# Kernel tuning notes

Hardware: AMD Instinct MI355X
Metric: run time of the kernel (lower is better)

## Reference

```python
import jax, jax.numpy as jnp
import numpy as np

N, E, D, K = 50000, 800000, 128, 128


def _graph_conv(x, src, dst, w, W_rel, b_rel, W_root, n_nodes):
    # PyG GraphConv (aggr='add'): out = lin_rel(sum_j w_ij * x_j) + lin_root(x)
    msg = w[:, None] * x[src]                              # [E, D]
    agg = jax.ops.segment_sum(msg, dst, num_segments=n_nodes)  # [N, D]
    return agg @ W_rel + b_rel + x @ W_root


def setup_inputs() -> dict:
    key = jax.random.key(0)
    ks = jax.random.split(key, 16)
    sc = 1.0 / np.sqrt(D).astype(np.float32)
    inp = {
        "x": jax.random.normal(ks[0], (N, D), dtype=jnp.float32),
        "edge_index": jax.random.randint(ks[1], (2, E), 0, N, dtype=jnp.int64 if jax.config.jax_enable_x64 else jnp.int32),
        "edge_weight": jax.random.uniform(ks[2], (E,), dtype=jnp.float32),
        # GraphConv layer 1
        "W_rel1": jax.random.normal(ks[3], (D, D), dtype=jnp.float32) * sc,
        "b_rel1": jnp.zeros((D,), dtype=jnp.float32),
        "W_root1": jax.random.normal(ks[4], (D, D), dtype=jnp.float32) * sc,
        # GraphConv layer 2
        "W_rel2": jax.random.normal(ks[5], (D, D), dtype=jnp.float32) * sc,
        "b_rel2": jnp.zeros((D,), dtype=jnp.float32),
        "W_root2": jax.random.normal(ks[6], (D, D), dtype=jnp.float32) * sc,
        # MLP: Linear(D,128) + Identity, then final Linear(128,K)
        "W_m1": jax.random.normal(ks[7], (D, 128), dtype=jnp.float32) * sc,
        "b_m1": jnp.zeros((128,), dtype=jnp.float32),
        "W_out": jax.random.normal(ks[8], (128, K), dtype=jnp.float32) * (1.0 / np.sqrt(128).astype(np.float32)),
        "b_out": jnp.zeros((K,), dtype=jnp.float32),
    }
    return inp


def reference(x, edge_index, edge_weight, W_rel1, b_rel1, W_root1,
              W_rel2, b_rel2, W_root2, W_m1, b_m1, W_out, b_out):
    n_nodes = x.shape[0]
    src, dst = edge_index[0], edge_index[1]

    # Message passing stack with ReLU
    h = jax.nn.relu(_graph_conv(x, src, dst, edge_weight, W_rel1, b_rel1, W_root1, n_nodes))
    h = jax.nn.relu(_graph_conv(h, src, dst, edge_weight, W_rel2, b_rel2, W_root2, n_nodes))

    # MLP -> cluster logits (mlp_act = Identity)
    s = (h @ W_m1 + b_m1) @ W_out + b_out                  # [N, K]
    probs = jax.nn.softmax(s, axis=-1)                     # [N, K]

    # dense_mincut_pool losses (computed edge-wise; A = to_dense_adj(edge_index, w))
    # degree d_i = sum_j A[i, j] = scatter of w over src
    deg = jax.ops.segment_sum(edge_weight, src, num_segments=n_nodes)  # [N]
    # mincut_num = trace(S^T A S) = sum_e w_e * <S[src_e], S[dst_e]>
    mincut_num = jnp.einsum('e,ek,ek->', edge_weight, probs[src], probs[dst])
    # mincut_den = trace(S^T D S) = sum_i d_i * ||S_i||^2
    mincut_den = jnp.sum(deg * jnp.sum(probs * probs, axis=-1))
    mc_loss = -(mincut_num / mincut_den)

    # orthogonality loss: || SS/||SS||_F - I/sqrt(K) ||_F
    ss = probs.T @ probs                                   # [K, K]
    k = probs.shape[1]
    o_loss = jnp.linalg.norm(ss / jnp.linalg.norm(ss) - jnp.eye(k, dtype=ss.dtype) / np.float32(np.sqrt(k)))

    return probs, mc_loss, o_loss
```

## Files before the change

kernel.cpp:

```cpp
#include <hip/hip_runtime.h>
#include <hip/hip_bf16.h>

#define D 128
#define KT 32
#define SS_BLOCKS 256
#define NUM_BLOCKS 2048

__device__ __forceinline__ float bfl(unsigned u) { return __uint_as_float(u << 16); }
__device__ __forceinline__ float bfh(unsigned u) { return __uint_as_float(u & 0xffff0000u); }

__global__ __launch_bounds__(256) void hist_deg_kernel(const int* __restrict__ src,
                                                       const int* __restrict__ dst,
                                                       const float* __restrict__ w,
                                                       int* __restrict__ cnt,
                                                       float* __restrict__ deg,
                                                       int* __restrict__ slot, int E) {
    int e = blockIdx.x * 256 + threadIdx.x;
    if (e < E) {
        slot[e] = atomicAdd(&cnt[dst[e]], 1);
        atomicAdd(&deg[src[e]], w[e]);
    }
}

__global__ __launch_bounds__(256) void scan_chunk_kernel(const int* __restrict__ cnt,
                                                         int* __restrict__ rowptr,
                                                         int* __restrict__ aux, int N) {
    __shared__ int ts[256];
    int t = threadIdx.x;
    int base = blockIdx.x * 1024 + t * 4;
    int v[4], s = 0;
#pragma unroll
    for (int i = 0; i < 4; ++i) {
        v[i] = (base + i < N) ? cnt[base + i] : 0;
        s += v[i];
    }
    ts[t] = s;
    __syncthreads();
#pragma unroll
    for (int off = 1; off < 256; off <<= 1) {
        int add = (t >= off) ? ts[t - off] : 0;
        __syncthreads();
        ts[t] += add;
        __syncthreads();
    }
    int run = ts[t] - s;
#pragma unroll
    for (int i = 0; i < 4; ++i) {
        run += v[i];
        if (base + i < N) rowptr[base + i + 1] = run;
    }
    if (t == 255) aux[blockIdx.x] = ts[255];
}

__global__ void scan_aux_kernel(int* __restrict__ aux, int nb) {
    if (threadIdx.x == 0) {
        int s = 0;
        for (int i = 0; i < nb; ++i) { s += aux[i]; aux[i] = s; }
    }
}

__global__ __launch_bounds__(256) void add_off_kernel(int* __restrict__ rowptr,
                                                      const int* __restrict__ aux, int N) {
    int i = blockIdx.x * 256 + threadIdx.x;
    if (i == 0) rowptr[0] = 0;
    if (i < N) {
        int b = i >> 10;
        if (b > 0) rowptr[i + 1] += aux[b - 1];
    }
}

__global__ __launch_bounds__(256) void fill_kernel(const int* __restrict__ src,
                                                   const int* __restrict__ dst,
                                                   const float* __restrict__ w,
                                                   const int* __restrict__ rowptr,
                                                   const int* __restrict__ slot,
                                                   int* __restrict__ csr_src,
                                                   float* __restrict__ csr_w, int E) {
    int e = blockIdx.x * 256 + threadIdx.x;
    if (e < E) {
        int pos = rowptr[dst[e]] + slot[e];
        csr_src[pos] = src[e];
        csr_w[pos] = w[e];
    }
}

#define ACC4(acc, we, v) { acc.x += (we) * (v).x; acc.y += (we) * (v).y; \
                           acc.z += (we) * (v).z; acc.w += (we) * (v).w; }

__global__ __launch_bounds__(256) void gather_kernel(const float* __restrict__ xin,
                                                     const int* __restrict__ csr_src,
                                                     const float* __restrict__ csr_w,
                                                     const int* __restrict__ rowptr,
                                                     float* __restrict__ agg, int N) {
    int node = blockIdx.x * 4 + (threadIdx.x >> 6);
    if (node >= N) return;
    int lane = threadIdx.x & 63;
    int half = lane >> 5;
    int c4 = (lane & 31) * 4;
    int beg = rowptr[node], end = rowptr[node + 1];
    float4 a[8];
#pragma unroll
    for (int i = 0; i < 8; ++i) a[i] = make_float4(0.f, 0.f, 0.f, 0.f);
    int j = beg;
    for (; j + 15 < end; j += 16) {
        int ei[8], si[8];
        float wi[8];
#pragma unroll
        for (int i = 0; i < 8; ++i) {
            ei[i] = j + 2 * i + half;
            si[i] = csr_src[ei[i]];
            wi[i] = csr_w[ei[i]];
        }
        float4 v[8];
#pragma unroll
        for (int i = 0; i < 8; ++i) v[i] = *(const float4*)&xin[(size_t)si[i] * D + c4];
#pragma unroll
        for (int i = 0; i < 8; ++i) ACC4(a[i], wi[i], v[i]);
    }
    for (; j + 7 < end; j += 8) {
#pragma unroll
        for (int i = 0; i < 4; ++i) {
            int e0 = j + 2 * i + half;
            int s0 = csr_src[e0]; float w0 = csr_w[e0];
            float4 v0 = *(const float4*)&xin[(size_t)s0 * D + c4];
            ACC4(a[i], w0, v0);
        }
    }
    for (; j + 1 < end; j += 2) {
        int e0 = j + half;
        int s0 = csr_src[e0]; float w0 = csr_w[e0];
        float4 v0 = *(const float4*)&xin[(size_t)s0 * D + c4];
        ACC4(a[0], w0, v0);
    }
    if (j < end && half == 0) {
        int s0 = csr_src[j]; float w0 = csr_w[j];
        float4 v0 = *(const float4*)&xin[(size_t)s0 * D + c4];
        ACC4(a[0], w0, v0);
    }
    float4 r = a[0];
#pragma unroll
    for (int i = 1; i < 8; ++i) { r.x += a[i].x; r.y += a[i].y; r.z += a[i].z; r.w += a[i].w; }
    r.x += __shfl_xor(r.x, 32);
    r.y += __shfl_xor(r.y, 32);
    r.z += __shfl_xor(r.z, 32);
    r.w += __shfl_xor(r.w, 32);
    if (half == 0) *(float4*)&agg[(size_t)node * D + c4] = r;
}

#define FMA4(acc, a, wv) { acc.x += (a) * (wv).x; acc.y += (a) * (wv).y; \
                           acc.z += (a) * (wv).z; acc.w += (a) * (wv).w; }

__global__ __launch_bounds__(256) void lin_kernel(const float* __restrict__ A1,
                                                  const float* __restrict__ A2,
                                                  const float* __restrict__ W1,
                                                  const float* __restrict__ W2,
                                                  const float* __restrict__ b,
                                                  float* __restrict__ out, int N) {
    __shared__ float As[KT][132];
    __shared__ float Ws[KT][D];
    int tid = threadIdx.x;
    int r0 = blockIdx.x * 128;
    int ty4 = (tid >> 3) * 4;
    int tx16 = (tid & 7) * 16;

    float4 acc[4][4];
#pragma unroll
    for (int i = 0; i < 4; ++i)
#pragma unroll
        for (int j = 0; j < 4; ++j) acc[i][j] = make_float4(0.f, 0.f, 0.f, 0.f);

    for (int t = 0; t < 8; ++t) {
        const float* A = (t < 4) ? A1 : A2;
        const float* W = (t < 4) ? W1 : W2;
        int koff = (t & 3) * KT;
        __syncthreads();
#pragma unroll
        for (int i = 0; i < 4; ++i) {
            int f4 = tid + i * 256;
            int row = f4 >> 3;
            int c4 = f4 & 7;
            float4 v = make_float4(0.f, 0.f, 0.f, 0.f);
            if (r0 + row < N) v = *(const float4*)&A[(size_t)(r0 + row) * D + koff + c4 * 4];
            As[c4 * 4 + 0][row] = v.x;
            As[c4 * 4 + 1][row] = v.y;
            As[c4 * 4 + 2][row] = v.z;
            As[c4 * 4 + 3][row] = v.w;
        }
#pragma unroll
        for (int i = 0; i < 4; ++i) {
            int f4 = tid + i * 256;
            int k = f4 >> 5;
            int c4 = f4 & 31;
            *(float4*)&Ws[k][c4 * 4] = *(const float4*)&W[(size_t)(koff + k) * D + c4 * 4];
        }
        __syncthreads();
#pragma unroll 4
        for (int k = 0; k < KT; ++k) {
            float4 av = *(const float4*)&As[k][ty4];
            float4 w0 = *(const float4*)&Ws[k][tx16];
            float4 w1 = *(const float4*)&Ws[k][tx16 + 4];
            float4 w2 = *(const float4*)&Ws[k][tx16 + 8];
            float4 w3 = *(const float4*)&Ws[k][tx16 + 12];
            FMA4(acc[0][0], av.x, w0); FMA4(acc[0][1], av.x, w1);
            FMA4(acc[0][2], av.x, w2); FMA4(acc[0][3], av.x, w3);
            FMA4(acc[1][0], av.y, w0); FMA4(acc[1][1], av.y, w1);
            FMA4(acc[1][2], av.y, w2); FMA4(acc[1][3], av.y, w3);
            FMA4(acc[2][0], av.z, w0); FMA4(acc[2][1], av.z, w1);
            FMA4(acc[2][2], av.z, w2); FMA4(acc[2][3], av.z, w3);
            FMA4(acc[3][0], av.w, w0); FMA4(acc[3][1], av.w, w1);
            FMA4(acc[3][2], av.w, w2); FMA4(acc[3][3], av.w, w3);
        }
    }
    float4 bv[4];
#pragma unroll
    for (int j = 0; j < 4; ++j) bv[j] = *(const float4*)&b[tx16 + j * 4];
#pragma unroll
    for (int i = 0; i < 4; ++i) {
        int r = r0 + ty4 + i;
        if (r < N) {
#pragma unroll
            for (int j = 0; j < 4; ++j) {
                float4 v;
                v.x = fmaxf(acc[i][j].x + bv[j].x, 0.f);
                v.y = fmaxf(acc[i][j].y + bv[j].y, 0.f);
                v.z = fmaxf(acc[i][j].z + bv[j].z, 0.f);
                v.w = fmaxf(acc[i][j].w + bv[j].w, 0.f);
                *(float4*)&out[(size_t)r * D + tx16 + j * 4] = v;
            }
        }
    }
}

__global__ __launch_bounds__(256) void smallmm_kernel(const float* __restrict__ Wm1,
                                                      const float* __restrict__ bm1,
                                                      const float* __restrict__ Wout,
                                                      const float* __restrict__ bout,
                                                      float* __restrict__ Wc,
                                                      float* __restrict__ bc) {
    int idx = blockIdx.x * 256 + threadIdx.x;
    if (blockIdx.x < 64) {
        int i = idx >> 7, j = idx & 127;
        float s = 0.f;
        for (int k = 0; k < 128; ++k) s += Wm1[i * 128 + k] * Wout[k * 128 + j];
        Wc[idx] = s;
    } else {
        int j = threadIdx.x;
        if (j < 128) {
            float s = bout[j];
            for (int k = 0; k < 128; ++k) s += bm1[k] * Wout[k * 128 + j];
            bc[j] = s;
        }
    }
}

__global__ __launch_bounds__(256) void out_softmax_kernel(const float* __restrict__ h2,
                                                          const float* __restrict__ Wc,
                                                          const float* __restrict__ bc,
                                                          const float* __restrict__ deg,
                                                          float* __restrict__ probs,
                                                          unsigned short* __restrict__ pbh,
                                                          float* __restrict__ accum, int N) {
    __shared__ float Rs[32][128];
    __shared__ float Ws[128 * 64];
    int tid = threadIdx.x;
    int wave = tid >> 6, lane = tid & 63;
    int r0 = blockIdx.x * 32;
#pragma unroll
    for (int i = 0; i < 4; ++i) {
        int f4 = tid + i * 256;
        int row = f4 >> 5;
        int c4 = f4 & 31;
        float4 v = make_float4(0.f, 0.f, 0.f, 0.f);
        if (r0 + row < N) v = *(const float4*)&h2[(size_t)(r0 + row) * D + c4 * 4];
        *(float4*)&Rs[row][c4 * 4] = v;
    }
    float lg[8][2];
#pragma unroll
    for (int h = 0; h < 2; ++h) {
        __syncthreads();
#pragma unroll
        for (int i = 0; i < 8; ++i) {
            int f4 = tid + i * 256;
            int k = f4 >> 4;
            int c4 = f4 & 15;
            *(float4*)&Ws[k * 64 + c4 * 4] = *(const float4*)&Wc[(size_t)k * 128 + h * 64 + c4 * 4];
        }
        __syncthreads();
        float bv = bc[h * 64 + lane];
        float a[8];
#pragma unroll
        for (int ri = 0; ri < 8; ++ri) a[ri] = bv;
        for (int k = 0; k < 128; ++k) {
            float wv = Ws[k * 64 + lane];
#pragma unroll
            for (int ri = 0; ri < 8; ++ri) a[ri] += Rs[wave + ri * 4][k] * wv;
        }
#pragma unroll
        for (int ri = 0; ri < 8; ++ri) lg[ri][h] = a[ri];
    }
    float den_local = 0.f;
#pragma unroll
    for (int ri = 0; ri < 8; ++ri) {
        int row = wave + ri * 4;
        int gr = r0 + row;
        float m = fmaxf(lg[ri][0], lg[ri][1]);
#pragma unroll
        for (int s = 32; s >= 1; s >>= 1) m = fmaxf(m, __shfl_xor(m, s));
        float e0 = expf(lg[ri][0] - m);
        float e1 = expf(lg[ri][1] - m);
        float sum = e0 + e1;
#pragma unroll
        for (int s = 32; s >= 1; s >>= 1) sum += __shfl_xor(sum, s);
        float inv = 1.f / sum;
        float p0 = e0 * inv, p1 = e1 * inv;
        float sq = p0 * p0 + p1 * p1;
#pragma unroll
        for (int s = 32; s >= 1; s >>= 1) sq += __shfl_xor(sq, s);
        if (gr < N) {
            probs[(size_t)gr * D + lane]      = p0;
            probs[(size_t)gr * D + 64 + lane] = p1;
            unsigned u0 = __float_as_uint(p0), u1 = __float_as_uint(p1);
            pbh[(size_t)gr * D + lane]      = (unsigned short)((u0 + 0x8000u) >> 16);
            pbh[(size_t)gr * D + 64 + lane] = (unsigned short)((u1 + 0x8000u) >> 16);
            if (lane == 0) den_local += deg[gr] * sq;
        }
    }
    if (lane == 0 && den_local != 0.f) atomicAdd(&accum[1], den_local);
}

__global__ __launch_bounds__(256) void num_ss_kernel(const float* __restrict__ probs,
                                                     const unsigned short* __restrict__ pbh,
                                                     const int* __restrict__ csr_src,
                                                     const float* __restrict__ csr_w,
                                                     const int* __restrict__ rowptr,
                                                     float* __restrict__ accum,
                                                     float* __restrict__ partial, int N) {
    int tid = threadIdx.x;
    if (blockIdx.x < SS_BLOCKS) {
        __shared__ float Ps[32][132];
        int a0 = (tid >> 4) * 8;
        int b0 = (tid & 15) * 8;
        float acc[8][8];
#pragma unroll
        for (int i = 0; i < 8; ++i)
#pragma unroll
            for (int j = 0; j < 8; ++j) acc[i][j] = 0.f;

        int rowsPerBlk = (N + SS_BLOCKS - 1) / SS_BLOCKS;
        int rbeg = blockIdx.x * rowsPerBlk;
        int rend = rbeg + rowsPerBlk;
        if (rend > N) rend = N;

        for (int c = rbeg; c < rend; c += 32) {
            int nr = rend - c;
            if (nr > 32) nr = 32;
            __syncthreads();
            for (int i = tid; i < nr * 32; i += 256) {
                int r = i >> 5, c4 = i & 31;
                *(float4*)&Ps[r][c4 * 4] = *(const float4*)&probs[(size_t)(c + r) * D + c4 * 4];
            }
            __syncthreads();
            for (int r = 0; r < nr; ++r) {
                float4 av0 = *(const float4*)&Ps[r][a0];
                float4 av1 = *(const float4*)&Ps[r][a0 + 4];
                float4 bv0 = *(const float4*)&Ps[r][b0];
                float4 bv1 = *(const float4*)&Ps[r][b0 + 4];
                float av[8] = {av0.x, av0.y, av0.z, av0.w, av1.x, av1.y, av1.z, av1.w};
                float bv[8] = {bv0.x, bv0.y, bv0.z, bv0.w, bv1.x, bv1.y, bv1.z, bv1.w};
#pragma unroll
                for (int i = 0; i < 8; ++i)
#pragma unroll
                    for (int j = 0; j < 8; ++j) acc[i][j] += av[i] * bv[j];
            }
        }
        float* pb = partial + (size_t)blockIdx.x * 16384;
#pragma unroll
        for (int i = 0; i < 8; ++i) {
            *(float4*)&pb[(a0 + i) * 128 + b0]     = make_float4(acc[i][0], acc[i][1], acc[i][2], acc[i][3]);
            *(float4*)&pb[(a0 + i) * 128 + b0 + 4] = make_float4(acc[i][4], acc[i][5], acc[i][6], acc[i][7]);
        }
        return;
    }
    int bid = blockIdx.x - SS_BLOCKS;
    int wave = tid >> 6, lane = tid & 63;
    int q = lane >> 4;
    int c8 = (lane & 15) * 8;
    float acc = 0.f;
    int stride = NUM_BLOCKS * 4;
    for (int node = bid * 4 + wave; node < N; node += stride) {
        float4 pdA = *(const float4*)&probs[(size_t)node * D + c8];
        float4 pdB = *(const float4*)&probs[(size_t)node * D + c8 + 4];
        int beg = rowptr[node], end = rowptr[node + 1];
        int j = beg;
        for (; j + 15 < end; j += 16) {
            int si[4]; float wi[4]; uint4 qv[4];
#pragma unroll
            for (int i = 0; i < 4; ++i) {
                int e = j + 4 * i + q;
                si[i] = csr_src[e];
                wi[i] = csr_w[e];
            }
#pragma unroll
            for (int i = 0; i < 4; ++i) qv[i] = *(const uint4*)&pbh[(size_t)si[i] * D + c8];
#pragma unroll
            for (int i = 0; i < 4; ++i) {
                acc += wi[i] * (bfl(qv[i].x) * pdA.x + bfh(qv[i].x) * pdA.y
                              + bfl(qv[i].y) * pdA.z + bfh(qv[i].y) * pdA.w
                              + bfl(qv[i].z) * pdB.x + bfh(qv[i].z) * pdB.y
                              + bfl(qv[i].w) * pdB.z + bfh(qv[i].w) * pdB.w);
            }
        }
        for (; j + 3 < end; j += 4) {
            int e = j + q;
            int s0 = csr_src[e]; float w0 = csr_w[e];
            uint4 qv = *(const uint4*)&pbh[(size_t)s0 * D + c8];
            acc += w0 * (bfl(qv.x) * pdA.x + bfh(qv.x) * pdA.y
                       + bfl(qv.y) * pdA.z + bfh(qv.y) * pdA.w
                       + bfl(qv.z) * pdB.x + bfh(qv.z) * pdB.y
                       + bfl(qv.w) * pdB.z + bfh(qv.w) * pdB.w);
        }
        int rem = end - j;
        if (q < rem) {
            int e = j + q;
            int s0 = csr_src[e]; float w0 = csr_w[e];
            uint4 qv = *(const uint4*)&pbh[(size_t)s0 * D + c8];
            acc += w0 * (bfl(qv.x) * pdA.x + bfh(qv.x) * pdA.y
                       + bfl(qv.y) * pdA.z + bfh(qv.y) * pdA.w
                       + bfl(qv.z) * pdB.x + bfh(qv.z) * pdB.y
                       + bfl(qv.w) * pdB.z + bfh(qv.w) * pdB.w);
        }
    }
#pragma unroll
    for (int m = 32; m >= 1; m >>= 1) acc += __shfl_xor(acc, m);
    if (lane == 0 && acc != 0.f) atomicAdd(&accum[0], acc);
}

__global__ __launch_bounds__(256) void ss_reduce_kernel(const float* __restrict__ partial,
                                                        float* __restrict__ ss) {
    int i = blockIdx.x * 256 + threadIdx.x;
    float s = 0.f;
    for (int b = 0; b < SS_BLOCKS; ++b) s += partial[(size_t)b * 16384 + i];
    ss[i] = s;
}

__global__ __launch_bounds__(256) void finalize_kernel(const float* __restrict__ ss,
                                                       const float* __restrict__ accum,
                                                       float* __restrict__ out2) {
    int tid = threadIdx.x;
    __shared__ float wsum[4], wsum2[4];
    float s = 0.f;
    for (int i = tid; i < 16384; i += 256) { float v = ss[i]; s += v * v; }
#pragma unroll
    for (int m = 32; m >= 1; m >>= 1) s += __shfl_xor(s, m);
    if ((tid & 63) == 0) wsum[tid >> 6] = s;
    __syncthreads();
    float norm = sqrtf(wsum[0] + wsum[1] + wsum[2] + wsum[3]);
    float inv = 1.f / norm;
    const float rk = 0.08838834764831845f;
    float o = 0.f;
    for (int i = tid; i < 16384; i += 256) {
        int a = i >> 7, b = i & 127;
        float v = ss[i] * inv - (a == b ? rk : 0.f);
        o += v * v;
    }
#pragma unroll
    for (int m = 32; m >= 1; m >>= 1) o += __shfl_xor(o, m);
    if ((tid & 63) == 0) wsum2[tid >> 6] = o;
    __syncthreads();
    if (tid == 0) {
        out2[0] = -(accum[0] / accum[1]);
        out2[1] = sqrtf(wsum2[0] + wsum2[1] + wsum2[2] + wsum2[3]);
    }
}

extern "C" void kernel_launch(void* const* d_in, const int* in_sizes, int n_in,
                              void* d_out, int out_size, void* d_ws, size_t ws_size,
                              hipStream_t stream) {
    const float* x      = (const float*)d_in[0];
    const int*   ei     = (const int*)d_in[1];
    const float* w      = (const float*)d_in[2];
    const float* Wrel1  = (const float*)d_in[3];
    const float* brel1  = (const float*)d_in[4];
    const float* Wroot1 = (const float*)d_in[5];
    const float* Wrel2  = (const float*)d_in[6];
    const float* brel2  = (const float*)d_in[7];
    const float* Wroot2 = (const float*)d_in[8];
    const float* Wm1    = (const float*)d_in[9];
    const float* bm1    = (const float*)d_in[10];
    const float* Wout   = (const float*)d_in[11];
    const float* bout   = (const float*)d_in[12];

    int N = in_sizes[0] / D;
    int E = in_sizes[2];
    const int* src = ei;
    const int* dst = ei + E;

    float* probs = (float*)d_out;
    float* out2  = probs + (size_t)N * D;
    float* h2    = probs;

    float* ws    = (float*)d_ws;
    float* agg   = ws;
    float* h1    = ws + (size_t)N * D;
    float* Wc    = ws + (size_t)2 * N * D;
    float* bc    = Wc + 16384;
    float* ssb   = bc + 128;
    float* deg   = ssb + 16384;
    float* accum = deg + N;
    float* csr_w = accum + 2;
    int*   cnt   = (int*)(csr_w + E);
    int*   rowptr= cnt + N;
    int*   aux   = rowptr + N + 1;
    int*   csr_src = aux + 64;
    int*   slot  = csr_src + E;

    unsigned short* pbh = (unsigned short*)h1;

    hipMemsetAsync(deg, 0, (size_t)(N + 2) * sizeof(float), stream);
    hipMemsetAsync(cnt, 0, (size_t)N * sizeof(int), stream);

    int eGrid = (E + 255) / 256;
    int nb = (N + 1023) / 1024;
    int linGrid = (N + 127) / 128;
    int nodeGrid = (N + 3) / 4;

    hist_deg_kernel<<<eGrid, 256, 0, stream>>>(src, dst, w, cnt, deg, slot, E);
    scan_chunk_kernel<<<nb, 256, 0, stream>>>(cnt, rowptr, aux, N);
    scan_aux_kernel<<<1, 64, 0, stream>>>(aux, nb);
    add_off_kernel<<<(N + 255) / 256, 256, 0, stream>>>(rowptr, aux, N);
    fill_kernel<<<eGrid, 256, 0, stream>>>(src, dst, w, rowptr, slot, csr_src, csr_w, E);

    gather_kernel<<<nodeGrid, 256, 0, stream>>>(x, csr_src, csr_w, rowptr, agg, N);
    lin_kernel<<<linGrid, 256, 0, stream>>>(agg, x, Wrel1, Wroot1, brel1, h1, N);
    gather_kernel<<<nodeGrid, 256, 0, stream>>>(h1, csr_src, csr_w, rowptr, agg, N);
    lin_kernel<<<linGrid, 256, 0, stream>>>(agg, h1, Wrel2, Wroot2, brel2, h2, N);
    smallmm_kernel<<<65, 256, 0, stream>>>(Wm1, bm1, Wout, bout, Wc, bc);
    out_softmax_kernel<<<(N + 31) / 32, 256, 0, stream>>>(h2, Wc, bc, deg, probs, pbh, accum, N);
    num_ss_kernel<<<SS_BLOCKS + NUM_BLOCKS, 256, 0, stream>>>(probs, pbh, csr_src, csr_w,
                                                              rowptr, accum, agg, N);
    ss_reduce_kernel<<<64, 256, 0, stream>>>(agg, ssb);
    finalize_kernel<<<1, 256, 0, stream>>>(ssb, accum, out2);
}
```

Baseline: 638.5 us.

## Fuse neighbor gather with GraphConv linear layer via shared-memory aggregate tile

Merges the CSR gather kernel and the dense linear kernel into one kernel per GraphConv layer. Each block gathers 64 nodes' aggregated features into shared memory and then multiplies them by W_rel, while the root term reads x tiles as before. This removes the agg round-trip through global memory and one launch per layer. The cost is a smaller row tile (64 instead of 128), more shared memory per block, which may lower occupancy, and serialized gather work per wave before the GEMM.

```diff
diff --git a/kernel.cpp b/kernel.cpp
--- a/kernel.cpp
+++ b/kernel.cpp
@@ -86,117 +86,122 @@
 
 #define ACC4(acc, we, v) { acc.x += (we) * (v).x; acc.y += (we) * (v).y; \
                            acc.z += (we) * (v).z; acc.w += (we) * (v).w; }
-
-__global__ __launch_bounds__(256) void gather_kernel(const float* __restrict__ xin,
-                                                     const int* __restrict__ csr_src,
-                                                     const float* __restrict__ csr_w,
-                                                     const int* __restrict__ rowptr,
-                                                     float* __restrict__ agg, int N) {
-    int node = blockIdx.x * 4 + (threadIdx.x >> 6);
-    if (node >= N) return;
-    int lane = threadIdx.x & 63;
+#define FMA4(acc, a, wv) { acc.x += (a) * (wv).x; acc.y += (a) * (wv).y; \
+                           acc.z += (a) * (wv).z; acc.w += (a) * (wv).w; }
+
+__global__ __launch_bounds__(256) void glin_kernel(const float* __restrict__ xin,
+                                                   const int* __restrict__ csr_src,
+                                                   const float* __restrict__ csr_w,
+                                                   const int* __restrict__ rowptr,
+                                                   const float* __restrict__ W1,
+                                                   const float* __restrict__ W2,
+                                                   const float* __restrict__ b,
+                                                   float* __restrict__ out, int N) {
+    __shared__ float Ag[D][68];
+    __shared__ float Ax[KT][68];
+    __shared__ float Ws[KT][D];
+    int tid = threadIdx.x;
+    int r0 = blockIdx.x * 64;
+    int wave = tid >> 6, lane = tid & 63;
     int half = lane >> 5;
     int c4 = (lane & 31) * 4;
-    int beg = rowptr[node], end = rowptr[node + 1];
-    float4 a[8];
-#pragma unroll
-    for (int i = 0; i < 8; ++i) a[i] = make_float4(0.f, 0.f, 0.f, 0.f);
-    int j = beg;
-    for (; j + 15 < end; j += 16) {
-        int ei[8], si[8];
-        float wi[8];
-#pragma unroll
-        for (int i = 0; i < 8; ++i) {
-            ei[i] = j + 2 * i + half;
-            si[i] = csr_src[ei[i]];
-            wi[i] = csr_w[ei[i]];
-        }
-        float4 v[8];
-#pragma unroll
-        for (int i = 0; i < 8; ++i) v[i] = *(const float4*)&xin[(size_t)si[i] * D + c4];
-#pragma unroll
-        for (int i = 0; i < 8; ++i) ACC4(a[i], wi[i], v[i]);
-    }
-    for (; j + 7 < end; j += 8) {
-#pragma unroll
-        for (int i = 0; i < 4; ++i) {
-            int e0 = j + 2 * i + half;
+
+    for (int nn = 0; nn < 16; ++nn) {
+        int row = wave + 4 * nn;
+        int node = r0 + row;
+        if (node >= N) break;
+        int beg = rowptr[node], end = rowptr[node + 1];
+        float4 a[8];
+#pragma unroll
+        for (int i = 0; i < 8; ++i) a[i] = make_float4(0.f, 0.f, 0.f, 0.f);
+        int j = beg;
+        for (; j + 15 < end; j += 16) {
+            int si[8]; float wi[8];
+#pragma unroll
+            for (int i = 0; i < 8; ++i) {
+                int e = j + 2 * i + half;
+                si[i] = csr_src[e];
+                wi[i] = csr_w[e];
+            }
+            float4 v[8];
+#pragma unroll
+            for (int i = 0; i < 8; ++i) v[i] = *(const float4*)&xin[(size_t)si[i] * D + c4];
+#pragma unroll
+            for (int i = 0; i < 8; ++i) ACC4(a[i], wi[i], v[i]);
+        }
+        for (; j + 7 < end; j += 8) {
+#pragma unroll
+            for (int i = 0; i < 4; ++i) {
+                int e0 = j + 2 * i + half;
+                int s0 = csr_src[e0]; float w0 = csr_w[e0];
+                float4 v0 = *(const float4*)&xin[(size_t)s0 * D + c4];
+                ACC4(a[i], w0, v0);
+            }
+        }
+        for (; j + 1 < end; j += 2) {
+            int e0 = j + half;
             int s0 = csr_src[e0]; float w0 = csr_w[e0];
             float4 v0 = *(const float4*)&xin[(size_t)s0 * D + c4];
-            ACC4(a[i], w0, v0);
-        }
-    }
-    for (; j + 1 < end; j += 2) {
-        int e0 = j + half;
-        int s0 = csr_src[e0]; float w0 = csr_w[e0];
-        float4 v0 = *(const float4*)&xin[(size_t)s0 * D + c4];
-        ACC4(a[0], w0, v0);
-    }
-    if (j < end && half == 0) {
-        int s0 = csr_src[j]; float w0 = csr_w[j];
-        float4 v0 = *(const float4*)&xin[(size_t)s0 * D + c4];
-        ACC4(a[0], w0, v0);
-    }
-    float4 r = a[0];
-#pragma unroll
-    for (int i = 1; i < 8; ++i) { r.x += a[i].x; r.y += a[i].y; r.z += a[i].z; r.w += a[i].w; }
-    r.x += __shfl_xor(r.x, 32);
-    r.y += __shfl_xor(r.y, 32);
-    r.z += __shfl_xor(r.z, 32);
-    r.w += __shfl_xor(r.w, 32);
-    if (half == 0) *(float4*)&agg[(size_t)node * D + c4] = r;
-}
-
-#define FMA4(acc, a, wv) { acc.x += (a) * (wv).x; acc.y += (a) * (wv).y; \
-                           acc.z += (a) * (wv).z; acc.w += (a) * (wv).w; }
-
-__global__ __launch_bounds__(256) void lin_kernel(const float* __restrict__ A1,
-                                                  const float* __restrict__ A2,
-                                                  const float* __restrict__ W1,
-                                                  const float* __restrict__ W2,
-                                                  const float* __restrict__ b,
-                                                  float* __restrict__ out, int N) {
-    __shared__ float As[KT][132];
-    __shared__ float Ws[KT][D];
-    int tid = threadIdx.x;
-    int r0 = blockIdx.x * 128;
-    int ty4 = (tid >> 3) * 4;
+            ACC4(a[0], w0, v0);
+        }
+        if (j < end && half == 0) {
+            int s0 = csr_src[j]; float w0 = csr_w[j];
+            float4 v0 = *(const float4*)&xin[(size_t)s0 * D + c4];
+            ACC4(a[0], w0, v0);
+        }
+        float4 r = a[0];
+#pragma unroll
+        for (int i = 1; i < 8; ++i) { r.x += a[i].x; r.y += a[i].y; r.z += a[i].z; r.w += a[i].w; }
+        r.x += __shfl_xor(r.x, 32);
+        r.y += __shfl_xor(r.y, 32);
+        r.z += __shfl_xor(r.z, 32);
+        r.w += __shfl_xor(r.w, 32);
+        if (half == 0) {
+            Ag[c4 + 0][row] = r.x;
+            Ag[c4 + 1][row] = r.y;
+            Ag[c4 + 2][row] = r.z;
+            Ag[c4 + 3][row] = r.w;
+        }
+    }
+
+    int ty2 = (tid >> 3) * 2;
     int tx16 = (tid & 7) * 16;
-
-    float4 acc[4][4];
-#pragma unroll
-    for (int i = 0; i < 4; ++i)
+    float4 acc[2][4];
+#pragma unroll
+    for (int i = 0; i < 2; ++i)
 #pragma unroll
         for (int j = 0; j < 4; ++j) acc[i][j] = make_float4(0.f, 0.f, 0.f, 0.f);
 
     for (int t = 0; t < 8; ++t) {
-        const float* A = (t < 4) ? A1 : A2;
         const float* W = (t < 4) ? W1 : W2;
         int koff = (t & 3) * KT;
         __syncthreads();
 #pragma unroll
         for (int i = 0; i < 4; ++i) {
             int f4 = tid + i * 256;
-            int row = f4 >> 3;
-            int c4 = f4 & 7;
-            float4 v = make_float4(0.f, 0.f, 0.f, 0.f);
-            if (r0 + row < N) v = *(const float4*)&A[(size_t)(r0 + row) * D + koff + c4 * 4];
-            As[c4 * 4 + 0][row] = v.x;
-            As[c4 * 4 + 1][row] = v.y;
-            As[c4 * 4 + 2][row] = v.z;
-            As[c4 * 4 + 3][row] = v.w;
-        }
-#pragma unroll
-        for (int i = 0; i < 4; ++i) {
-            int f4 = tid + i * 256;
             int k = f4 >> 5;
-            int c4 = f4 & 31;
-            *(float4*)&Ws[k][c4 * 4] = *(const float4*)&W[(size_t)(koff + k) * D + c4 * 4];
+            int cc = f4 & 31;
+            *(float4*)&Ws[k][cc * 4] = *(const float4*)&W[(size_t)(koff + k) * D + cc * 4];
+        }
+        if (t >= 4) {
+#pragma unroll
+            for (int i = 0; i < 2; ++i) {
+                int f4 = tid + i * 256;
+                int row = f4 >> 3;
+                int cq = f4 & 7;
+                float4 v = make_float4(0.f, 0.f, 0.f, 0.f);
+                if (r0 + row < N) v = *(const float4*)&xin[(size_t)(r0 + row) * D + koff + cq * 4];
+                Ax[cq * 4 + 0][row] = v.x;
+                Ax[cq * 4 + 1][row] = v.y;
+                Ax[cq * 4 + 2][row] = v.z;
+                Ax[cq * 4 + 3][row] = v.w;
+            }
         }
         __syncthreads();
+        const float* Ab = (t < 4) ? &Ag[koff][0] : &Ax[0][0];
 #pragma unroll 4
         for (int k = 0; k < KT; ++k) {
-            float4 av = *(const float4*)&As[k][ty4];
+            float2 av = *(const float2*)&Ab[k * 68 + ty2];
             float4 w0 = *(const float4*)&Ws[k][tx16];
             float4 w1 = *(const float4*)&Ws[k][tx16 + 4];
             float4 w2 = *(const float4*)&Ws[k][tx16 + 8];
@@ -205,18 +210,14 @@
             FMA4(acc[0][2], av.x, w2); FMA4(acc[0][3], av.x, w3);
             FMA4(acc[1][0], av.y, w0); FMA4(acc[1][1], av.y, w1);
             FMA4(acc[1][2], av.y, w2); FMA4(acc[1][3], av.y, w3);
-            FMA4(acc[2][0], av.z, w0); FMA4(acc[2][1], av.z, w1);
-            FMA4(acc[2][2], av.z, w2); FMA4(acc[2][3], av.z, w3);
-            FMA4(acc[3][0], av.w, w0); FMA4(acc[3][1], av.w, w1);
-            FMA4(acc[3][2], av.w, w2); FMA4(acc[3][3], av.w, w3);
         }
     }
     float4 bv[4];
 #pragma unroll
     for (int j = 0; j < 4; ++j) bv[j] = *(const float4*)&b[tx16 + j * 4];
 #pragma unroll
-    for (int i = 0; i < 4; ++i) {
-        int r = r0 + ty4 + i;
+    for (int i = 0; i < 2; ++i) {
+        int r = r0 + ty2 + i;
         if (r < N) {
 #pragma unroll
             for (int j = 0; j < 4; ++j) {
@@ -521,8 +522,7 @@
 
     int eGrid = (E + 255) / 256;
     int nb = (N + 1023) / 1024;
-    int linGrid = (N + 127) / 128;
-    int nodeGrid = (N + 3) / 4;
+    int glinGrid = (N + 63) / 64;
 
     hist_deg_kernel<<<eGrid, 256, 0, stream>>>(src, dst, w, cnt, deg, slot, E);
     scan_chunk_kernel<<<nb, 256, 0, stream>>>(cnt, rowptr, aux, N);
@@ -530,10 +530,10 @@
     add_off_kernel<<<(N + 255) / 256, 256, 0, stream>>>(rowptr, aux, N);
     fill_kernel<<<eGrid, 256, 0, stream>>>(src, dst, w, rowptr, slot, csr_src, csr_w, E);
 
-    gather_kernel<<<nodeGrid, 256, 0, stream>>>(x, csr_src, csr_w, rowptr, agg, N);
-    lin_kernel<<<linGrid, 256, 0, stream>>>(agg, x, Wrel1, Wroot1, brel1, h1, N);
-    gather_kernel<<<nodeGrid, 256, 0, stream>>>(h1, csr_src, csr_w, rowptr, agg, N);
-    lin_kernel<<<linGrid, 256, 0, stream>>>(agg, h1, Wrel2, Wroot2, brel2, h2, N);
+    glin_kernel<<<glinGrid, 256, 0, stream>>>(x, csr_src, csr_w, rowptr,
+                                              Wrel1, Wroot1, brel1, h1, N);
+    glin_kernel<<<glinGrid, 256, 0, stream>>>(h1, csr_src, csr_w, rowptr,
+                                              Wrel2, Wroot2, brel2, h2, N);
     smallmm_kernel<<<65, 256, 0, stream>>>(Wm1, bm1, Wout, bout, Wc, bc);
     out_softmax_kernel<<<(N + 31) / 32, 256, 0, stream>>>(h2, Wc, bc, deg, probs, pbh, accum, N);
     num_ss_kernel<<<SS_BLOCKS + NUM_BLOCKS, 256, 0, stream>>>(probs, pbh, csr_src, csr_w,
```

After: 724.8 us. +13.5%, slower.

## Gather layer-1 from bf16 copy of x and fuse layer-2 linear with softmax

Applied to the files above, without the earlier changes.

Adds a kernel that converts x to bf16 so the first edge gather reads half the bytes per neighbor row, using a new 16-lane-per-edge gather with fp32 accumulation. It also fuses the second GraphConv linear (rel+root, bias, ReLU) with the MLP/softmax stage, keeping h2 tiles in shared memory instead of writing and rereading them. The bf16 rounding of x changes the numerics of the first aggregation. The workspace layout moves pbh to a new region, and the fused kernel reads Wc directly from global memory instead of staging it in shared memory.

```diff
diff --git a/kernel.cpp b/kernel.cpp
--- a/kernel.cpp
+++ b/kernel.cpp
@@ -8,6 +8,23 @@
 
 __device__ __forceinline__ float bfl(unsigned u) { return __uint_as_float(u << 16); }
 __device__ __forceinline__ float bfh(unsigned u) { return __uint_as_float(u & 0xffff0000u); }
+__device__ __forceinline__ unsigned short f2b(float f) {
+    unsigned u = __float_as_uint(f);
+    return (unsigned short)((u + 0x7fffu + ((u >> 16) & 1u)) >> 16);
+}
+
+__global__ __launch_bounds__(256) void f2bf_kernel(const float* __restrict__ in,
+                                                   unsigned short* __restrict__ out, int n8) {
+    int i = blockIdx.x * 256 + threadIdx.x;
+    if (i < n8) {
+        float4 a = ((const float4*)in)[2 * i];
+        float4 b = ((const float4*)in)[2 * i + 1];
+        ushort4 lo = make_ushort4(f2b(a.x), f2b(a.y), f2b(a.z), f2b(a.w));
+        ushort4 hi = make_ushort4(f2b(b.x), f2b(b.y), f2b(b.z), f2b(b.w));
+        ((ushort4*)out)[2 * i] = lo;
+        ((ushort4*)out)[2 * i + 1] = hi;
+    }
+}
 
 __global__ __launch_bounds__(256) void hist_deg_kernel(const int* __restrict__ src,
                                                        const int* __restrict__ dst,
@@ -84,6 +101,73 @@
     }
 }
 
+__global__ __launch_bounds__(256) void gatherq_kernel(const unsigned short* __restrict__ xh,
+                                                      const int* __restrict__ csr_src,
+                                                      const float* __restrict__ csr_w,
+                                                      const int* __restrict__ rowptr,
+                                                      float* __restrict__ agg, int N) {
+    int node = blockIdx.x * 4 + (threadIdx.x >> 6);
+    if (node >= N) return;
+    int lane = threadIdx.x & 63;
+    int q = lane >> 4;
+    int c8 = (lane & 15) * 8;
+    int beg = rowptr[node], end = rowptr[node + 1];
+    float a[4][8];
+#pragma unroll
+    for (int i = 0; i < 4; ++i)
+#pragma unroll
+        for (int k = 0; k < 8; ++k) a[i][k] = 0.f;
+    int j = beg;
+    for (; j + 15 < end; j += 16) {
+        int si[4]; float wi[4]; uint4 qv[4];
+#pragma unroll
+        for (int i = 0; i < 4; ++i) {
+            int e = j + 4 * i + q;
+            si[i] = csr_src[e];
+            wi[i] = csr_w[e];
+        }
+#pragma unroll
+        for (int i = 0; i < 4; ++i) qv[i] = *(const uint4*)&xh[(size_t)si[i] * D + c8];
+#pragma unroll
+        for (int i = 0; i < 4; ++i) {
+            a[i][0] += wi[i] * bfl(qv[i].x); a[i][1] += wi[i] * bfh(qv[i].x);
+            a[i][2] += wi[i] * bfl(qv[i].y); a[i][3] += wi[i] * bfh(qv[i].y);
+            a[i][4] += wi[i] * bfl(qv[i].z); a[i][5] += wi[i] * bfh(qv[i].z);
+            a[i][6] += wi[i] * bfl(qv[i].w); a[i][7] += wi[i] * bfh(qv[i].w);
+        }
+    }
+    for (; j + 3 < end; j += 4) {
+        int e = j + q;
+        int s0 = csr_src[e]; float w0 = csr_w[e];
+        uint4 qv = *(const uint4*)&xh[(size_t)s0 * D + c8];
+        a[0][0] += w0 * bfl(qv.x); a[0][1] += w0 * bfh(qv.x);
+        a[0][2] += w0 * bfl(qv.y); a[0][3] += w0 * bfh(qv.y);
+        a[0][4] += w0 * bfl(qv.z); a[0][5] += w0 * bfh(qv.z);
+        a[0][6] += w0 * bfl(qv.w); a[0][7] += w0 * bfh(qv.w);
+    }
+    int rem = end - j;
+    if (q < rem) {
+        int e = j + q;
+        int s0 = csr_src[e]; float w0 = csr_w[e];
+        uint4 qv = *(const uint4*)&xh[(size_t)s0 * D + c8];
+        a[1][0] += w0 * bfl(qv.x); a[1][1] += w0 * bfh(qv.x);
+        a[1][2] += w0 * bfl(qv.y); a[1][3] += w0 * bfh(qv.y);
+        a[1][4] += w0 * bfl(qv.z); a[1][5] += w0 * bfh(qv.z);
+        a[1][6] += w0 * bfl(qv.w); a[1][7] += w0 * bfh(qv.w);
+    }
+    float r[8];
+#pragma unroll
+    for (int k = 0; k < 8; ++k) {
+        r[k] = a[0][k] + a[1][k] + a[2][k] + a[3][k];
+        r[k] += __shfl_xor(r[k], 16);
+        r[k] += __shfl_xor(r[k], 32);
+    }
+    if (lane < 16) {
+        *(float4*)&agg[(size_t)node * D + c8]     = make_float4(r[0], r[1], r[2], r[3]);
+        *(float4*)&agg[(size_t)node * D + c8 + 4] = make_float4(r[4], r[5], r[6], r[7]);
+    }
+}
+
 #define ACC4(acc, we, v) { acc.x += (we) * (v).x; acc.y += (we) * (v).y; \
                            acc.z += (we) * (v).z; acc.w += (we) * (v).w; }
 
@@ -103,13 +187,12 @@
     for (int i = 0; i < 8; ++i) a[i] = make_float4(0.f, 0.f, 0.f, 0.f);
     int j = beg;
     for (; j + 15 < end; j += 16) {
-        int ei[8], si[8];
-        float wi[8];
+        int si[8]; float wi[8];
 #pragma unroll
         for (int i = 0; i < 8; ++i) {
-            ei[i] = j + 2 * i + half;
-            si[i] = csr_src[ei[i]];
-            wi[i] = csr_w[ei[i]];
+            int e = j + 2 * i + half;
+            si[i] = csr_src[e];
+            wi[i] = csr_w[e];
         }
         float4 v[8];
 #pragma unroll
@@ -253,61 +336,113 @@
     }
 }
 
-__global__ __launch_bounds__(256) void out_softmax_kernel(const float* __restrict__ h2,
-                                                          const float* __restrict__ Wc,
-                                                          const float* __restrict__ bc,
-                                                          const float* __restrict__ deg,
-                                                          float* __restrict__ probs,
-                                                          unsigned short* __restrict__ pbh,
-                                                          float* __restrict__ accum, int N) {
-    __shared__ float Rs[32][128];
-    __shared__ float Ws[128 * 64];
+__global__ __launch_bounds__(256) void lin2sm_kernel(const float* __restrict__ A1,
+                                                     const float* __restrict__ A2,
+                                                     const float* __restrict__ W1,
+                                                     const float* __restrict__ W2,
+                                                     const float* __restrict__ b,
+                                                     const float* __restrict__ Wc,
+                                                     const float* __restrict__ bc,
+                                                     const float* __restrict__ deg,
+                                                     float* __restrict__ probs,
+                                                     unsigned short* __restrict__ pbh,
+                                                     float* __restrict__ accum, int N) {
+    __shared__ float As[KT][68];
+    __shared__ float Ws[KT][D];
+    __shared__ float Rs[64][132];
     int tid = threadIdx.x;
+    int r0 = blockIdx.x * 64;
+    int ty2 = (tid >> 3) * 2;
+    int tx16 = (tid & 7) * 16;
+
+    float4 acc[2][4];
+#pragma unroll
+    for (int i = 0; i < 2; ++i)
+#pragma unroll
+        for (int j = 0; j < 4; ++j) acc[i][j] = make_float4(0.f, 0.f, 0.f, 0.f);
+
+    for (int t = 0; t < 8; ++t) {
+        const float* A = (t < 4) ? A1 : A2;
+        const float* W = (t < 4) ? W1 : W2;
+        int koff = (t & 3) * KT;
+        __syncthreads();
+#pragma unroll
+        for (int i = 0; i < 2; ++i) {
+            int f4 = tid + i * 256;
+            int row = f4 >> 3;
+            int cq = f4 & 7;
+            float4 v = make_float4(0.f, 0.f, 0.f, 0.f);
+            if (r0 + row < N) v = *(const float4*)&A[(size_t)(r0 + row) * D + koff + cq * 4];
+            As[cq * 4 + 0][row] = v.x;
+            As[cq * 4 + 1][row] = v.y;
+            As[cq * 4 + 2][row] = v.z;
+            As[cq * 4 + 3][row] = v.w;
+        }
+#pragma unroll
+        for (int i = 0; i < 4; ++i) {
+            int f4 = tid + i * 256;
+            int k = f4 >> 5;
+            int cc = f4 & 31;
+            *(float4*)&Ws[k][cc * 4] = *(const float4*)&W[(size_t)(koff + k) * D + cc * 4];
+        }
+        __syncthreads();
+#pragma unroll 4
+        for (int k = 0; k < KT; ++k) {
+            float2 av = *(const float2*)&As[k][ty2];
+            float4 w0 = *(const float4*)&Ws[k][tx16];
+            float4 w1 = *(const float4*)&Ws[k][tx16 + 4];
+            float4 w2 = *(const float4*)&Ws[k][tx16 + 8];
+            float4 w3 = *(const float4*)&Ws[k][tx16 + 12];
+            FMA4(acc[0][0], av.x, w0); FMA4(acc[0][1], av.x, w1);
+            FMA4(acc[0][2], av.x, w2); FMA4(acc[0][3], av.x, w3);
+            FMA4(acc[1][0], av.y, w0); FMA4(acc[1][1], av.y, w1);
+            FMA4(acc[1][2], av.y, w2); FMA4(acc[1][3], av.y, w3);
+        }
+    }
+    float4 bv[4];
+#pragma unroll
+    for (int j = 0; j < 4; ++j) bv[j] = *(const float4*)&b[tx16 + j * 4];
+#pragma unroll
+    for (int i = 0; i < 2; ++i) {
+#pragma unroll
+        for (int j = 0; j < 4; ++j) {
+            float4 v;
+            v.x = fmaxf(acc[i][j].x + bv[j].x, 0.f);
+            v.y = fmaxf(acc[i][j].y + bv[j].y, 0.f);
+            v.z = fmaxf(acc[i][j].z + bv[j].z, 0.f);
+            v.w = fmaxf(acc[i][j].w + bv[j].w, 0.f);
+            *(float4*)&Rs[ty2 + i][tx16 + j * 4] = v;
+        }
+    }
+    __syncthreads();
+
     int wave = tid >> 6, lane = tid & 63;
-    int r0 = blockIdx.x * 32;
-#pragma unroll
-    for (int i = 0; i < 4; ++i) {
-        int f4 = tid + i * 256;
-        int row = f4 >> 5;
-        int c4 = f4 & 31;
-        float4 v = make_float4(0.f, 0.f, 0.f, 0.f);
-        if (r0 + row < N) v = *(const float4*)&h2[(size_t)(r0 + row) * D + c4 * 4];
-        *(float4*)&Rs[row][c4 * 4] = v;
-    }
-    float lg[8][2];
+    float lg[16][2];
 #pragma unroll
     for (int h = 0; h < 2; ++h) {
-        __syncthreads();
-#pragma unroll
-        for (int i = 0; i < 8; ++i) {
-            int f4 = tid + i * 256;
-            int k = f4 >> 4;
-            int c4 = f4 & 15;
-            *(float4*)&Ws[k * 64 + c4 * 4] = *(const float4*)&Wc[(size_t)k * 128 + h * 64 + c4 * 4];
-        }
-        __syncthreads();
-        float bv = bc[h * 64 + lane];
-        float a[8];
-#pragma unroll
-        for (int ri = 0; ri < 8; ++ri) a[ri] = bv;
+        float bvh = bc[h * 64 + lane];
+        float a2[16];
+#pragma unroll
+        for (int rr = 0; rr < 16; ++rr) a2[rr] = bvh;
+#pragma unroll 4
         for (int k = 0; k < 128; ++k) {
-            float wv = Ws[k * 64 + lane];
-#pragma unroll
-            for (int ri = 0; ri < 8; ++ri) a[ri] += Rs[wave + ri * 4][k] * wv;
-        }
-#pragma unroll
-        for (int ri = 0; ri < 8; ++ri) lg[ri][h] = a[ri];
+            float wv = Wc[k * 128 + h * 64 + lane];
+#pragma unroll
+            for (int rr = 0; rr < 16; ++rr) a2[rr] += Rs[wave + rr * 4][k] * wv;
+        }
+#pragma unroll
+        for (int rr = 0; rr < 16; ++rr) lg[rr][h] = a2[rr];
     }
     float den_local = 0.f;
 #pragma unroll
-    for (int ri = 0; ri < 8; ++ri) {
-        int row = wave + ri * 4;
+    for (int rr = 0; rr < 16; ++rr) {
+        int row = wave + rr * 4;
         int gr = r0 + row;
-        float m = fmaxf(lg[ri][0], lg[ri][1]);
+        float m = fmaxf(lg[rr][0], lg[rr][1]);
 #pragma unroll
         for (int s = 32; s >= 1; s >>= 1) m = fmaxf(m, __shfl_xor(m, s));
-        float e0 = expf(lg[ri][0] - m);
-        float e1 = expf(lg[ri][1] - m);
+        float e0 = expf(lg[rr][0] - m);
+        float e1 = expf(lg[rr][1] - m);
         float sum = e0 + e1;
 #pragma unroll
         for (int s = 32; s >= 1; s >>= 1) sum += __shfl_xor(sum, s);
@@ -319,9 +454,8 @@
         if (gr < N) {
             probs[(size_t)gr * D + lane]      = p0;
             probs[(size_t)gr * D + 64 + lane] = p1;
-            unsigned u0 = __float_as_uint(p0), u1 = __float_as_uint(p1);
-            pbh[(size_t)gr * D + lane]      = (unsigned short)((u0 + 0x8000u) >> 16);
-            pbh[(size_t)gr * D + 64 + lane] = (unsigned short)((u1 + 0x8000u) >> 16);
+            pbh[(size_t)gr * D + lane]      = f2b(p0);
+            pbh[(size_t)gr * D + 64 + lane] = f2b(p1);
             if (lane == 0) den_local += deg[gr] * sq;
         }
     }
@@ -497,7 +631,6 @@
 
     float* probs = (float*)d_out;
     float* out2  = probs + (size_t)N * D;
-    float* h2    = probs;
 
     float* ws    = (float*)d_ws;
     float* agg   = ws;
@@ -513,16 +646,17 @@
     int*   aux   = rowptr + N + 1;
     int*   csr_src = aux + 64;
     int*   slot  = csr_src + E;
-
-    unsigned short* pbh = (unsigned short*)h1;
+    unsigned short* pbh = (unsigned short*)(slot + E);
+    unsigned short* xh  = (unsigned short*)h1;
 
     hipMemsetAsync(deg, 0, (size_t)(N + 2) * sizeof(float), stream);
     hipMemsetAsync(cnt, 0, (size_t)N * sizeof(int), stream);
 
     int eGrid = (E + 255) / 256;
     int nb = (N + 1023) / 1024;
-    int linGrid = (N + 127) / 128;
-    int nodeGrid = (N + 3) / 4;
+    int n8 = N * D / 8;
+
+    f2bf_kernel<<<(n8 + 255) / 256, 256, 0, stream>>>(x, xh, n8);
 
     hist_deg_kernel<<<eGrid, 256, 0, stream>>>(src, dst, w, cnt, deg, slot, E);
     scan_chunk_kernel<<<nb, 256, 0, stream>>>(cnt, rowptr, aux, N);
@@ -530,12 +664,12 @@
     add_off_kernel<<<(N + 255) / 256, 256, 0, stream>>>(rowptr, aux, N);
     fill_kernel<<<eGrid, 256, 0, stream>>>(src, dst, w, rowptr, slot, csr_src, csr_w, E);
 
-    gather_kernel<<<nodeGrid, 256, 0, stream>>>(x, csr_src, csr_w, rowptr, agg, N);
-    lin_kernel<<<linGrid, 256, 0, stream>>>(agg, x, Wrel1, Wroot1, brel1, h1, N);
-    gather_kernel<<<nodeGrid, 256, 0, stream>>>(h1, csr_src, csr_w, rowptr, agg, N);
-    lin_kernel<<<linGrid, 256, 0, stream>>>(agg, h1, Wrel2, Wroot2, brel2, h2, N);
+    gatherq_kernel<<<(N + 3) / 4, 256, 0, stream>>>(xh, csr_src, csr_w, rowptr, agg, N);
+    lin_kernel<<<(N + 127) / 128, 256, 0, stream>>>(agg, x, Wrel1, Wroot1, brel1, h1, N);
+    gather_kernel<<<(N + 3) / 4, 256, 0, stream>>>(h1, csr_src, csr_w, rowptr, agg, N);
     smallmm_kernel<<<65, 256, 0, stream>>>(Wm1, bm1, Wout, bout, Wc, bc);
-    out_softmax_kernel<<<(N + 31) / 32, 256, 0, stream>>>(h2, Wc, bc, deg, probs, pbh, accum, N);
+    lin2sm_kernel<<<(N + 63) / 64, 256, 0, stream>>>(agg, h1, Wrel2, Wroot2, brel2,
+                                                     Wc, bc, deg, probs, pbh, accum, N);
     num_ss_kernel<<<SS_BLOCKS + NUM_BLOCKS, 256, 0, stream>>>(probs, pbh, csr_src, csr_w,
                                                               rowptr, accum, agg, N);
     ss_reduce_kernel<<<64, 256, 0, stream>>>(agg, ssb);
```

New measurement: 627.2 us. No clear change (-1.8%).

## Gather neighbor features from bf16 copies in both GraphConv aggregations

Applied to the files above, without the earlier changes.

A new pass converts x to a bf16 copy, and the first linear layer also writes a bf16 copy of h1. Both edge-gather aggregations then read these 16-bit rows, each lane loading eight features, and accumulate in fp32. This halves the bytes fetched per gathered neighbor row, which is the main traffic of the message passing. The costs are an extra conversion pass, an extra bf16 store in lin_kernel, a new workspace region for pbh (which assumes the workspace is large enough), and reduced precision in the aggregated features. Bf16 rounding also switches to round-to-nearest-even.

```diff
diff --git a/kernel.cpp b/kernel.cpp
--- a/kernel.cpp
+++ b/kernel.cpp
@@ -8,6 +8,23 @@
 
 __device__ __forceinline__ float bfl(unsigned u) { return __uint_as_float(u << 16); }
 __device__ __forceinline__ float bfh(unsigned u) { return __uint_as_float(u & 0xffff0000u); }
+__device__ __forceinline__ unsigned short f2b(float f) {
+    unsigned u = __float_as_uint(f);
+    return (unsigned short)((u + 0x7fffu + ((u >> 16) & 1u)) >> 16);
+}
+
+__global__ __launch_bounds__(256) void f2bf_kernel(const float* __restrict__ in,
+                                                   unsigned short* __restrict__ out, int n8) {
+    int i = blockIdx.x * 256 + threadIdx.x;
+    if (i < n8) {
+        float4 a = ((const float4*)in)[2 * i];
+        float4 b = ((const float4*)in)[2 * i + 1];
+        ushort4 lo = make_ushort4(f2b(a.x), f2b(a.y), f2b(a.z), f2b(a.w));
+        ushort4 hi = make_ushort4(f2b(b.x), f2b(b.y), f2b(b.z), f2b(b.w));
+        ((ushort4*)out)[2 * i] = lo;
+        ((ushort4*)out)[2 * i + 1] = hi;
+    }
+}
 
 __global__ __launch_bounds__(256) void hist_deg_kernel(const int* __restrict__ src,
                                                        const int* __restrict__ dst,
@@ -84,67 +101,71 @@
     }
 }
 
-#define ACC4(acc, we, v) { acc.x += (we) * (v).x; acc.y += (we) * (v).y; \
-                           acc.z += (we) * (v).z; acc.w += (we) * (v).w; }
-
-__global__ __launch_bounds__(256) void gather_kernel(const float* __restrict__ xin,
-                                                     const int* __restrict__ csr_src,
-                                                     const float* __restrict__ csr_w,
-                                                     const int* __restrict__ rowptr,
-                                                     float* __restrict__ agg, int N) {
+__global__ __launch_bounds__(256) void gatherq_kernel(const unsigned short* __restrict__ xh,
+                                                      const int* __restrict__ csr_src,
+                                                      const float* __restrict__ csr_w,
+                                                      const int* __restrict__ rowptr,
+                                                      float* __restrict__ agg, int N) {
     int node = blockIdx.x * 4 + (threadIdx.x >> 6);
     if (node >= N) return;
     int lane = threadIdx.x & 63;
-    int half = lane >> 5;
-    int c4 = (lane & 31) * 4;
+    int q = lane >> 4;
+    int c8 = (lane & 15) * 8;
     int beg = rowptr[node], end = rowptr[node + 1];
-    float4 a[8];
-#pragma unroll
-    for (int i = 0; i < 8; ++i) a[i] = make_float4(0.f, 0.f, 0.f, 0.f);
+    float a[4][8];
+#pragma unroll
+    for (int i = 0; i < 4; ++i)
+#pragma unroll
+        for (int k = 0; k < 8; ++k) a[i][k] = 0.f;
     int j = beg;
     for (; j + 15 < end; j += 16) {
-        int ei[8], si[8];
-        float wi[8];
-#pragma unroll
-        for (int i = 0; i < 8; ++i) {
-            ei[i] = j + 2 * i + half;
-            si[i] = csr_src[ei[i]];
-            wi[i] = csr_w[ei[i]];
-        }
-        float4 v[8];
-#pragma unroll
-        for (int i = 0; i < 8; ++i) v[i] = *(const float4*)&xin[(size_t)si[i] * D + c4];
-#pragma unroll
-        for (int i = 0; i < 8; ++i) ACC4(a[i], wi[i], v[i]);
-    }
-    for (; j + 7 < end; j += 8) {
+        int si[4]; float wi[4]; uint4 qv[4];
 #pragma unroll
         for (int i = 0; i < 4; ++i) {
-            int e0 = j + 2 * i + half;
-            int s0 = csr_src[e0]; float w0 = csr_w[e0];
-            float4 v0 = *(const float4*)&xin[(size_t)s0 * D + c4];
-            ACC4(a[i], w0, v0);
-        }
-    }
-    for (; j + 1 < end; j += 2) {
-        int e0 = j + half;
-        int s0 = csr_src[e0]; float w0 = csr_w[e0];
-        float4 v0 = *(const float4*)&xin[(size_t)s0 * D + c4];
-        ACC4(a[0], w0, v0);
-    }
-    if (j < end && half == 0) {
-        int s0 = csr_src[j]; float w0 = csr_w[j];
-        float4 v0 = *(const float4*)&xin[(size_t)s0 * D + c4];
-        ACC4(a[0], w0, v0);
-    }
-    float4 r = a[0];
-#pragma unroll
-    for (int i = 1; i < 8; ++i) { r.x += a[i].x; r.y += a[i].y; r.z += a[i].z; r.w += a[i].w; }
-    r.x += __shfl_xor(r.x, 32);
-    r.y += __shfl_xor(r.y, 32);
-    r.z += __shfl_xor(r.z, 32);
-    r.w += __shfl_xor(r.w, 32);
-    if (half == 0) *(float4*)&agg[(size_t)node * D + c4] = r;
+            int e = j + 4 * i + q;
+            si[i] = csr_src[e];
+            wi[i] = csr_w[e];
+        }
+#pragma unroll
+        for (int i = 0; i < 4; ++i) qv[i] = *(const uint4*)&xh[(size_t)si[i] * D + c8];
+#pragma unroll
+        for (int i = 0; i < 4; ++i) {
+            a[i][0] += wi[i] * bfl(qv[i].x); a[i][1] += wi[i] * bfh(qv[i].x);
+            a[i][2] += wi[i] * bfl(qv[i].y); a[i][3] += wi[i] * bfh(qv[i].y);
+            a[i][4] += wi[i] * bfl(qv[i].z); a[i][5] += wi[i] * bfh(qv[i].z);
+            a[i][6] += wi[i] * bfl(qv[i].w); a[i][7] += wi[i] * bfh(qv[i].w);
+        }
+    }
+    for (; j + 3 < end; j += 4) {
+        int e = j + q;
+        int s0 = csr_src[e]; float w0 = csr_w[e];
+        uint4 qv = *(const uint4*)&xh[(size_t)s0 * D + c8];
+        a[0][0] += w0 * bfl(qv.x); a[0][1] += w0 * bfh(qv.x);
+        a[0][2] += w0 * bfl(qv.y); a[0][3] += w0 * bfh(qv.y);
+        a[0][4] += w0 * bfl(qv.z); a[0][5] += w0 * bfh(qv.z);
+        a[0][6] += w0 * bfl(qv.w); a[0][7] += w0 * bfh(qv.w);
+    }
+    int rem = end - j;
+    if (q < rem) {
+        int e = j + q;
+        int s0 = csr_src[e]; float w0 = csr_w[e];
+        uint4 qv = *(const uint4*)&xh[(size_t)s0 * D + c8];
+        a[1][0] += w0 * bfl(qv.x); a[1][1] += w0 * bfh(qv.x);
+        a[1][2] += w0 * bfl(qv.y); a[1][3] += w0 * bfh(qv.y);
+        a[1][4] += w0 * bfl(qv.z); a[1][5] += w0 * bfh(qv.z);
+        a[1][6] += w0 * bfl(qv.w); a[1][7] += w0 * bfh(qv.w);
+    }
+    float r[8];
+#pragma unroll
+    for (int k = 0; k < 8; ++k) {
+        r[k] = a[0][k] + a[1][k] + a[2][k] + a[3][k];
+        r[k] += __shfl_xor(r[k], 16);
+        r[k] += __shfl_xor(r[k], 32);
+    }
+    if (lane < 16) {
+        *(float4*)&agg[(size_t)node * D + c8]     = make_float4(r[0], r[1], r[2], r[3]);
+        *(float4*)&agg[(size_t)node * D + c8 + 4] = make_float4(r[4], r[5], r[6], r[7]);
+    }
 }
 
 #define FMA4(acc, a, wv) { acc.x += (a) * (wv).x; acc.y += (a) * (wv).y; \
@@ -155,7 +176,8 @@
                                                   const float* __restrict__ W1,
                                                   const float* __restrict__ W2,
                                                   const float* __restrict__ b,
-                                                  float* __restrict__ out, int N) {
+                                                  float* __restrict__ out,
+                                                  unsigned short* __restrict__ outh, int N) {
     __shared__ float As[KT][132];
     __shared__ float Ws[KT][D];
     int tid = threadIdx.x;
@@ -226,6 +248,10 @@
                 v.z = fmaxf(acc[i][j].z + bv[j].z, 0.f);
                 v.w = fmaxf(acc[i][j].w + bv[j].w, 0.f);
                 *(float4*)&out[(size_t)r * D + tx16 + j * 4] = v;
+                if (outh) {
+                    ushort4 u = make_ushort4(f2b(v.x), f2b(v.y), f2b(v.z), f2b(v.w));
+                    *(ushort4*)&outh[(size_t)r * D + tx16 + j * 4] = u;
+                }
             }
         }
     }
@@ -319,9 +345,8 @@
         if (gr < N) {
             probs[(size_t)gr * D + lane]      = p0;
             probs[(size_t)gr * D + 64 + lane] = p1;
-            unsigned u0 = __float_as_uint(p0), u1 = __float_as_uint(p1);
-            pbh[(size_t)gr * D + lane]      = (unsigned short)((u0 + 0x8000u) >> 16);
-            pbh[(size_t)gr * D + 64 + lane] = (unsigned short)((u1 + 0x8000u) >> 16);
+            pbh[(size_t)gr * D + lane]      = f2b(p0);
+            pbh[(size_t)gr * D + 64 + lane] = f2b(p1);
             if (lane == 0) den_local += deg[gr] * sq;
         }
     }
@@ -513,16 +538,17 @@
     int*   aux   = rowptr + N + 1;
     int*   csr_src = aux + 64;
     int*   slot  = csr_src + E;
-
-    unsigned short* pbh = (unsigned short*)h1;
+    unsigned short* pbh = (unsigned short*)(slot + E);
+    unsigned short* xh  = (unsigned short*)h1;
 
     hipMemsetAsync(deg, 0, (size_t)(N + 2) * sizeof(float), stream);
     hipMemsetAsync(cnt, 0, (size_t)N * sizeof(int), stream);
 
     int eGrid = (E + 255) / 256;
     int nb = (N + 1023) / 1024;
-    int linGrid = (N + 127) / 128;
-    int nodeGrid = (N + 3) / 4;
+    int n8 = N * D / 8;
+
+    f2bf_kernel<<<(n8 + 255) / 256, 256, 0, stream>>>(x, xh, n8);
 
     hist_deg_kernel<<<eGrid, 256, 0, stream>>>(src, dst, w, cnt, deg, slot, E);
     scan_chunk_kernel<<<nb, 256, 0, stream>>>(cnt, rowptr, aux, N);
@@ -530,10 +556,12 @@
     add_off_kernel<<<(N + 255) / 256, 256, 0, stream>>>(rowptr, aux, N);
     fill_kernel<<<eGrid, 256, 0, stream>>>(src, dst, w, rowptr, slot, csr_src, csr_w, E);
 
-    gather_kernel<<<nodeGrid, 256, 0, stream>>>(x, csr_src, csr_w, rowptr, agg, N);
-    lin_kernel<<<linGrid, 256, 0, stream>>>(agg, x, Wrel1, Wroot1, brel1, h1, N);
-    gather_kernel<<<nodeGrid, 256, 0, stream>>>(h1, csr_src, csr_w, rowptr, agg, N);
-    lin_kernel<<<linGrid, 256, 0, stream>>>(agg, h1, Wrel2, Wroot2, brel2, h2, N);
+    gatherq_kernel<<<(N + 3) / 4, 256, 0, stream>>>(xh, csr_src, csr_w, rowptr, agg, N);
+    lin_kernel<<<(N + 127) / 128, 256, 0, stream>>>(agg, x, Wrel1, Wroot1, brel1,
+                                                    h1, pbh, N);
+    gatherq_kernel<<<(N + 3) / 4, 256, 0, stream>>>(pbh, csr_src, csr_w, rowptr, agg, N);
+    lin_kernel<<<(N + 127) / 128, 256, 0, stream>>>(agg, h1, Wrel2, Wroot2, brel2,
+                                                    h2, (unsigned short*)nullptr, N);
     smallmm_kernel<<<65, 256, 0, stream>>>(Wm1, bm1, Wout, bout, Wc, bc);
     out_softmax_kernel<<<(N + 31) / 32, 256, 0, stream>>>(h2, Wc, bc, deg, probs, pbh, accum, N);
     num_ss_kernel<<<SS_BLOCKS + NUM_BLOCKS, 256, 0, stream>>>(probs, pbh, csr_src, csr_w,
```

New measurement: 620.2 us. 2.9% less time.
